# Kernel optimization log

Measured on AMD Instinct MI355X. Metric: run time of the kernel, lower is better.

Reference implementation:

```python
import jax, jax.numpy as jnp
import numpy as np

B, IMG, P, CIN = 4, 384, 16, 3
G = IMG // P            # 24 patches per side
NP = G * G              # 576 patch tokens
N = NP + 1              # +cls
D, H, L, MLP, NC = 768, 12, 12, 3072, 1000
HD = D // H
SCALE = HD ** -0.5
NUM_REL = (2 * G - 1) * (2 * G - 1) + 3   # (2*1-1)*(2G-1)*(2G-1)+3 = 2212
EPS = 1e-6


def gen_rel_index():
    # window (1, G, G): depth diff is always 0, reduces to 2D BEiT indexing
    coords = np.stack(np.meshgrid(np.arange(G), np.arange(G), indexing='ij')).reshape(2, -1)
    rel = (coords[:, :, None] - coords[:, None, :]).transpose(1, 2, 0).copy()  # (NP,NP,2)
    rel[:, :, 0] += G - 1
    rel[:, :, 1] += G - 1
    rel[:, :, 0] *= 2 * G - 1
    idx = np.zeros((N, N), dtype=np.int32)
    idx[1:, 1:] = rel.sum(-1)
    idx[0, :] = NUM_REL - 3
    idx[:, 0] = NUM_REL - 2
    idx[0, 0] = NUM_REL - 1
    return jnp.asarray(idx)


def setup_inputs() -> dict:
    key = jax.random.key(0)
    ks = jax.random.split(key, 20)
    s = 0.02
    inp = {
        'x': jax.random.normal(ks[0], (B, CIN, IMG, IMG), jnp.float32),
        'patch_w': s * jax.random.normal(ks[1], (D, CIN * P * P), jnp.float32),
        'patch_b': jnp.zeros((D,), jnp.float32),
        'cls_token': s * jax.random.normal(ks[2], (1, 1, D), jnp.float32),
        'pos_embed': s * jax.random.normal(ks[3], (1, N, D), jnp.float32),
        'ln1_w': jnp.ones((L, D), jnp.float32),
        'ln1_b': jnp.zeros((L, D), jnp.float32),
        'qkv_w': s * jax.random.normal(ks[4], (L, 3 * D, D), jnp.float32),
        'q_bias': jnp.zeros((L, D), jnp.float32),
        'v_bias': jnp.zeros((L, D), jnp.float32),
        'proj_w': s * jax.random.normal(ks[5], (L, D, D), jnp.float32),
        'proj_b': jnp.zeros((L, D), jnp.float32),
        'ln2_w': jnp.ones((L, D), jnp.float32),
        'ln2_b': jnp.zeros((L, D), jnp.float32),
        'fc1_w': s * jax.random.normal(ks[6], (L, MLP, D), jnp.float32),
        'fc1_b': jnp.zeros((L, MLP), jnp.float32),
        'fc2_w': s * jax.random.normal(ks[7], (L, D, MLP), jnp.float32),
        'fc2_b': jnp.zeros((L, D), jnp.float32),
        'rel_table': s * jax.random.normal(ks[8], (L, NUM_REL, H), jnp.float32),
        'fc_norm_w': jnp.ones((D,), jnp.float32),
        'fc_norm_b': jnp.zeros((D,), jnp.float32),
        'head_w': s * jax.random.normal(ks[9], (NC, D), jnp.float32),
        'head_b': jnp.zeros((NC,), jnp.float32),
        'rel_index': gen_rel_index(),
    }
    return inp


def _ln(x, w, b):
    m = x.mean(-1, keepdims=True)
    v = ((x - m) ** 2).mean(-1, keepdims=True)
    return (x - m) * jax.lax.rsqrt(v + EPS) * w + b


def _beit_fwd(x, patch_w, patch_b, cls_token, pos_embed,
              ln1_w, ln1_b, qkv_w, q_bias, v_bias, proj_w, proj_b,
              ln2_w, ln2_b, fc1_w, fc1_b, fc2_w, fc2_b, rel_table,
              fc_norm_w, fc_norm_b, head_w, head_b, rel_index):
    # patch embed: conv P x P stride P == reshape + matmul; patch vec order (c, ph, pw)
    patches = x.reshape(B, CIN, G, P, G, P).transpose(0, 2, 4, 1, 3, 5).reshape(B, NP, CIN * P * P)
    tok = patches @ patch_w.T + patch_b                      # (B, NP, D)
    h = jnp.concatenate([jnp.broadcast_to(cls_token, (B, 1, D)), tok], axis=1) + pos_embed

    def block(h, p):
        l1w, l1b, qw, qb, vb, pw, pb, l2w, l2b, f1w, f1b, f2w, f2b, rt = p
        y = _ln(h, l1w, l1b)
        bias = jnp.concatenate([qb, jnp.zeros_like(qb), vb])  # k_bias frozen zeros
        qkv = (y @ qw.T + bias).reshape(B, N, 3, H, HD).transpose(2, 0, 3, 1, 4)
        q, k, v = qkv[0] * SCALE, qkv[1], qkv[2]              # (B,H,N,HD)
        attn = jnp.einsum('bhnd,bhmd->bhnm', q, k)
        rel = rt[rel_index].transpose(2, 0, 1)                # (H,N,N)
        attn = jax.nn.softmax(attn + rel[None], axis=-1)
        o = jnp.einsum('bhnm,bhmd->bhnd', attn, v).transpose(0, 2, 1, 3).reshape(B, N, D)
        h = h + (o @ pw.T + pb)
        y = _ln(h, l2w, l2b)
        y = jax.nn.gelu(y @ f1w.T + f1b, approximate=False) @ f2w.T + f2b
        return h + y, None

    xs = (ln1_w, ln1_b, qkv_w, q_bias, v_bias, proj_w, proj_b,
          ln2_w, ln2_b, fc1_w, fc1_b, fc2_w, fc2_b, rel_table)
    h, _ = jax.lax.scan(block, h, xs)

    pooled = h[:, 1:].mean(axis=1)                            # global_pool='avg' drops cls
    return _ln(pooled, fc_norm_w, fc_norm_b) @ head_w.T + head_b  # (B, NC)


def reference(x, patch_w, patch_b, cls_token, pos_embed,
              ln1_w, ln1_b, qkv_w, q_bias, v_bias, proj_w, proj_b,
              ln2_w, ln2_b, fc1_w, fc1_b, fc2_w, fc2_b, rel_table,
              fc_norm_w, fc_norm_b, head_w, head_b, rel_index):
    return _beit_fwd(x, patch_w, patch_b, cls_token, pos_embed,
                     ln1_w, ln1_b, qkv_w, q_bias, v_bias, proj_w, proj_b,
                     ln2_w, ln2_b, fc1_w, fc1_b, fc2_w, fc2_b, rel_table,
                     fc_norm_w, fc_norm_b, head_w, head_b, rel_index)
```

## Files before the change

kernel.cpp:

```cpp
#include <hip/hip_runtime.h>
#include <math.h>

typedef unsigned short u16;
typedef __bf16 bf16x8_t __attribute__((ext_vector_type(8)));
typedef u16 u16x8 __attribute__((ext_vector_type(8)));
typedef float f32x4 __attribute__((ext_vector_type(4)));

#define CBATCH 4
#define CN 577
#define CNP 576
#define CD 768
#define CH 12
#define CHD 64
#define CL 12
#define CMLP 3072
#define CVP 640
#define CROWS (CBATCH*CN)
#define CROWSP 2432
#define CNN2 332929
#define CBH (CBATCH*CH)
#define CSK 4
#define CMT 37

__device__ __forceinline__ float b2f(u16 u){
  unsigned x = ((unsigned)u) << 16;
  return __builtin_bit_cast(float, x);
}
__device__ __forceinline__ u16 f2b(float f){
  unsigned x = __builtin_bit_cast(unsigned, f);
  unsigned r = x + 0x7fffu + ((x >> 16) & 1u);
  return (u16)(r >> 16);
}

__device__ __forceinline__ f32x4 MFMA(u16x8 a, u16x8 b, f32x4 c){
  return __builtin_amdgcn_mfma_f32_16x16x32_bf16(
      __builtin_bit_cast(bf16x8_t, a), __builtin_bit_cast(bf16x8_t, b), c, 0, 0, 0);
}

__device__ __forceinline__ void gl_lds16(const u16* g, u16* l){
  __builtin_amdgcn_global_load_lds(
      (const __attribute__((address_space(1))) unsigned int*)g,
      (__attribute__((address_space(3))) unsigned int*)l, 16, 0, 0);
}


__global__ void cvt_kernel(const float* __restrict__ src, u16* __restrict__ dst, int n){
  int i = (blockIdx.x * 256 + threadIdx.x) * 4;
  if(i < n){
    float4 v = *reinterpret_cast<const float4*>(src + i);
    ushort4 o;
    o.x = f2b(v.x); o.y = f2b(v.y); o.z = f2b(v.z); o.w = f2b(v.w);
    *reinterpret_cast<ushort4*>(dst + i) = o;
  }
}

__global__ void zero_kernel(u16* __restrict__ p, int n){
  int i = (blockIdx.x * 256 + threadIdx.x) * 8;
  if(i < n){
    u16x8 z = {0,0,0,0,0,0,0,0};
    *reinterpret_cast<u16x8*>(p + i) = z;
  }
}

__global__ void im2col_kernel(const float* __restrict__ x, u16* __restrict__ out){
  int id = blockIdx.x * 256 + threadIdx.x;
  if(id >= 2304*768) return;
  int col = id % 768, row = id / 768;
  int b = row / 576, p = row % 576;
  int gy = p / 24, gx = p % 24;
  int c = col >> 8, rem = col & 255, py = rem >> 4, px = rem & 15;
  float v = x[(((long)(b*3 + c)*384) + gy*16 + py)*384 + gx*16 + px];
  out[id] = f2b(v);
}

__global__ void clspos_kernel(const float* __restrict__ cls, const float* __restrict__ pos,
                              float* __restrict__ h){
  int id = blockIdx.x * 256 + threadIdx.x;
  if(id < CBATCH*CD){
    int b = id / CD, d = id % CD;
    h[(long)b*CN*CD + d] = cls[d] + pos[d];
  }
}

template<bool BF16OUT>
__global__ void ln_kernel(const float* __restrict__ x, const float* __restrict__ w,
                          const float* __restrict__ bsh, u16* __restrict__ yb,
                          float* __restrict__ yf){
  int r = blockIdx.x;
  int tid = threadIdx.x;
  const float* px = x + (long)r*CD;
  float v0 = px[tid], v1 = px[tid+256], v2 = px[tid+512];
  __shared__ float red[4];
  float s = v0 + v1 + v2;
  #pragma unroll
  for(int m=1;m<64;m<<=1) s += __shfl_xor(s, m);
  if((tid & 63) == 0) red[tid>>6] = s;
  __syncthreads();
  s = red[0]+red[1]+red[2]+red[3];
  float mean = s * (1.0f/768.0f);
  float d0 = v0-mean, d1 = v1-mean, d2 = v2-mean;
  float s2 = d0*d0 + d1*d1 + d2*d2;
  __syncthreads();
  #pragma unroll
  for(int m=1;m<64;m<<=1) s2 += __shfl_xor(s2, m);
  if((tid & 63) == 0) red[tid>>6] = s2;
  __syncthreads();
  s2 = red[0]+red[1]+red[2]+red[3];
  float rs = rsqrtf(s2*(1.0f/768.0f) + 1e-6f);
  float o0 = d0*rs*w[tid]     + bsh[tid];
  float o1 = d1*rs*w[tid+256] + bsh[tid+256];
  float o2 = d2*rs*w[tid+512] + bsh[tid+512];
  if(BF16OUT){
    yb[(long)r*CD + tid]     = f2b(o0);
    yb[(long)r*CD + tid+256] = f2b(o1);
    yb[(long)r*CD + tid+512] = f2b(o2);
  } else {
    yf[(long)r*CD + tid]     = o0;
    yf[(long)r*CD + tid+256] = o1;
    yf[(long)r*CD + tid+512] = o2;
  }
}

template<bool DOLN>
__global__ void resid_ln_kernel(float* __restrict__ h, const float* __restrict__ part,
    const float* __restrict__ bias, const float* __restrict__ w,
    const float* __restrict__ bsh, u16* __restrict__ y){
  int r = blockIdx.x, tid = threadIdx.x;
  float v[3];
  #pragma unroll
  for(int j=0;j<3;j++){
    int c = tid + j*256;
    float t = h[(long)r*CD + c] + bias[c];
    #pragma unroll
    for(int sk=0; sk<CSK; sk++) t += part[((long)sk*CROWS + r)*CD + c];
    v[j] = t;
    h[(long)r*CD + c] = t;
  }
  if constexpr(DOLN){
    __shared__ float red[4];
    float s = v[0]+v[1]+v[2];
    #pragma unroll
    for(int m=1;m<64;m<<=1) s += __shfl_xor(s, m);
    if((tid & 63) == 0) red[tid>>6] = s;
    __syncthreads();
    s = red[0]+red[1]+red[2]+red[3];
    float mean = s * (1.0f/768.0f);
    float d0=v[0]-mean, d1=v[1]-mean, d2=v[2]-mean;
    float s2 = d0*d0+d1*d1+d2*d2;
    __syncthreads();
    #pragma unroll
    for(int m=1;m<64;m<<=1) s2 += __shfl_xor(s2, m);
    if((tid & 63) == 0) red[tid>>6] = s2;
    __syncthreads();
    s2 = red[0]+red[1]+red[2]+red[3];
    float rs = rsqrtf(s2*(1.0f/768.0f) + 1e-6f);
    y[(long)r*CD + tid]     = f2b(d0*rs*w[tid]     + bsh[tid]);
    y[(long)r*CD + tid+256] = f2b(d1*rs*w[tid+256] + bsh[tid+256]);
    y[(long)r*CD + tid+512] = f2b(d2*rs*w[tid+512] + bsh[tid+512]);
  }
}

__global__ void relbias_all_kernel(const int* __restrict__ ridx, const float* __restrict__ rtab,
                                   u16* __restrict__ attb){
  int id = blockIdx.x * 256 + threadIdx.x;
  if(id >= CNN2) return;
  int l = blockIdx.y;
  int idx = ridx[id];
  const float* rowp = rtab + (long)l*2212*12 + (long)idx*12;
  u16* dst = attb + (long)l*12*CNN2;
  #pragma unroll
  for(int hh=0; hh<12; hh++)
    dst[(long)hh*CNN2 + id] = f2b(rowp[hh]);
}

__global__ __launch_bounds__(256) void attn_kernel(
    const u16* __restrict__ q, const u16* __restrict__ k,
    const u16* __restrict__ vt, const u16* __restrict__ attb,
    u16* __restrict__ o_){
  __shared__ u16 pt[4][16*72];
  const int tid = threadIdx.x, lane = tid & 63, wv = tid >> 6;
  const int i15 = lane & 15, g4 = lane >> 4;
  const int qt = blockIdx.x, bh = blockIdx.y;
  const int b = bh / CH, hh = bh % CH;
  const int qrow0 = qt*64 + wv*16;
  const u16* qp = q + ((long)bh*CN + qrow0 + i15)*CHD + g4*8;
  u16x8 qa0 = *reinterpret_cast<const u16x8*>(qp);
  u16x8 qa1 = *reinterpret_cast<const u16x8*>(qp + 32);
  const u16* kbase = k + (long)bh*CN*CHD;
  const u16* vbase = vt + (long)bh*CHD*CVP;
  const u16* bb = attb + (long)hh*CNN2;
  f32x4 po[4];
  float m[4], l[4];
  #pragma unroll
  for(int i=0;i<4;i++){ po[i]=(f32x4){0,0,0,0}; m[i]=-3.0e38f; l[i]=0.0f; }

  for(int t=0;t<10;t++){
    const int kv0 = t*64;
    f32x4 sa[4];
    #pragma unroll
    for(int fc=0;fc<4;fc++){
      const u16* kp = kbase + ((long)(kv0 + fc*16 + i15))*CHD + g4*8;
      u16x8 k0 = *reinterpret_cast<const u16x8*>(kp);
      u16x8 k1 = *reinterpret_cast<const u16x8*>(kp + 32);
      f32x4 z = (f32x4){0,0,0,0};
      z = MFMA(qa0, k0, z);
      z = MFMA(qa1, k1, z);
      sa[fc] = z;
    }
    float s[4][4];
    #pragma unroll
    for(int fc=0;fc<4;fc++){
      int kvc = kv0 + fc*16 + i15;
      bool valid = kvc < CN;
      #pragma unroll
      for(int r=0;r<4;r++){
        int qr = qrow0 + g4*4 + r;
        float bias = b2f(bb[(long)qr*CN + kvc]);
        s[fc][r] = valid ? (sa[fc][r] + bias) : -1e30f;
      }
    }
    float tm[4], ts[4], sc[4];
    #pragma unroll
    for(int r=0;r<4;r++)
      tm[r] = fmaxf(fmaxf(s[0][r],s[1][r]), fmaxf(s[2][r],s[3][r]));
    #pragma unroll
    for(int msk=1; msk<16; msk<<=1)
      #pragma unroll
      for(int r=0;r<4;r++)
        tm[r] = fmaxf(tm[r], __shfl_xor(tm[r], msk));
    #pragma unroll
    for(int r=0;r<4;r++){
      float mn = fmaxf(m[r], tm[r]);
      sc[r] = exp2f((m[r]-mn)*1.4426950408889634f);
      m[r] = mn;
      ts[r] = 0.f;
    }
    #pragma unroll
    for(int fc=0;fc<4;fc++)
      #pragma unroll
      for(int r=0;r<4;r++){
        float p = exp2f((s[fc][r]-m[r])*1.4426950408889634f);
        s[fc][r] = p; ts[r] += p;
      }
    #pragma unroll
    for(int msk=1; msk<16; msk<<=1)
      #pragma unroll
      for(int r=0;r<4;r++)
        ts[r] += __shfl_xor(ts[r], msk);
    #pragma unroll
    for(int r=0;r<4;r++) l[r] = l[r]*sc[r] + ts[r];
    #pragma unroll
    for(int d=0; d<4; d++)
      #pragma unroll
      for(int r=0;r<4;r++) po[d][r] *= sc[r];
    #pragma unroll
    for(int fc=0;fc<4;fc++)
      #pragma unroll
      for(int r=0;r<4;r++)
        pt[wv][(g4*4+r)*72 + fc*16 + i15] = f2b(s[fc][r]);
    u16x8 pa0 = *reinterpret_cast<const u16x8*>(&pt[wv][i15*72 + g4*8]);
    u16x8 pa1 = *reinterpret_cast<const u16x8*>(&pt[wv][i15*72 + 32 + g4*8]);
    #pragma unroll
    for(int d=0; d<4; d++){
      const u16* vp = vbase + ((long)(d*16 + i15))*CVP + kv0 + g4*8;
      u16x8 v0 = *reinterpret_cast<const u16x8*>(vp);
      u16x8 v1 = *reinterpret_cast<const u16x8*>(vp + 32);
      po[d] = MFMA(pa0, v0, po[d]);
      po[d] = MFMA(pa1, v1, po[d]);
    }
  }
  #pragma unroll
  for(int d=0; d<4; d++)
    #pragma unroll
    for(int r=0;r<4;r++){
      int qr = qrow0 + g4*4 + r;
      if(qr < CN)
        o_[((long)(b*CN + qr))*CD + hh*CHD + d*16 + i15] = f2b(po[d][r] / l[r]);
    }
}

__global__ void pool_kernel(const float* __restrict__ h, float* __restrict__ pooled){
  int id = blockIdx.x * 256 + threadIdx.x;
  if(id >= CBATCH*CD) return;
  int b = id / CD, d = id % CD;
  const float* p = h + ((long)b*CN + 1)*CD + d;
  float s = 0.0f;
  for(int i=0;i<CNP;i++) s += p[(long)i*CD];
  pooled[id] = s * (1.0f/576.0f);
}

__global__ void head_kernel(const float* __restrict__ xn, const float* __restrict__ hw,
                            const float* __restrict__ hb, float* __restrict__ out){
  int nc = blockIdx.x;
  int tid = threadIdx.x;
  const float* wr = hw + (long)nc*CD;
  float w0 = wr[tid], w1 = wr[tid+256], w2 = wr[tid+512];
  __shared__ float red[4];
  for(int b=0;b<CBATCH;b++){
    const float* xr = xn + (long)b*CD;
    float s = w0*xr[tid] + w1*xr[tid+256] + w2*xr[tid+512];
    #pragma unroll
    for(int m=1;m<64;m<<=1) s += __shfl_xor(s, m);
    if((tid&63)==0) red[tid>>6] = s;
    __syncthreads();
    if(tid==0) out[b*1000 + nc] = red[0]+red[1]+red[2]+red[3] + hb[nc];
    __syncthreads();
  }
}


struct EpiArgs {
  float* hres;
  u16* outb;
  const float* bias;
  const float* pos;
  const float* qb;
  const float* vb;
  u16* q;
  u16* k;
  u16* vt;
  float* part;
};

enum { EPI_PATCH=0, EPI_QKV, EPI_GELU, EPI_PART };

template<int EPI>
__global__ __launch_bounds__(256,4) void gemm4(const u16* __restrict__ A, const u16* __restrict__ Bm,
    int M, int N, int K, int lda, int ldb, EpiArgs e){
  __shared__ __align__(16) u16 lA[3][64*32];
  __shared__ __align__(16) u16 lB[3][128*32];
  const int tid  = threadIdx.x;
  const int lane = tid & 63;
  const int wv   = tid >> 6;

  const int bm = blockIdx.y * 64, bn = blockIdx.x * 128;
  const int z  = blockIdx.z;
  A  += (long)z * K;
  Bm += (long)z * K;

  const int srow = wv*16 + (lane>>2);
  const u16* Asb = A  + (long)(bm + srow)*lda + (lane&3)*8;
  const u16* Bsb = Bm + (long)(bn + srow)*ldb + (lane&3)*8;
  const int ldst = wv*16*32;

  const int rbase = (wv>>1)*32;
  const int cbase = (wv&1)*64;
  const int i15 = lane & 15;
  const int k8off = (lane>>4)<<3;

  f32x4 acc[2][4];
  #pragma unroll
  for(int i=0;i<2;i++)
    #pragma unroll
    for(int j=0;j<4;j++)
      acc[i][j] = (f32x4){0.0f,0.0f,0.0f,0.0f};

  const int nkt = K >> 5;

  auto STAGE = [&](int kt, int slot){
    const u16* Ak = Asb + (long)kt*32;
    const u16* Bk = Bsb + (long)kt*32;
    gl_lds16(Ak,          &lA[slot][ldst]);
    gl_lds16(Bk,          &lB[slot][ldst]);
    gl_lds16(Bk + 64*ldb, &lB[slot][ldst + 64*32]);
  };

  STAGE(0, 0);
  if(nkt > 1) STAGE(1, 1);

  for(int kt=0; kt<nkt; kt++){
    if(kt+1 < nkt) asm volatile("s_waitcnt vmcnt(3) lgkmcnt(0)" ::: "memory");
    else           asm volatile("s_waitcnt vmcnt(0) lgkmcnt(0)" ::: "memory");
    __builtin_amdgcn_s_barrier();
    int nxt2 = kt + 2; 
    if(nxt2 < nkt){ int sl = nxt2 % 3; STAGE(nxt2, sl); }
    const int cur = kt % 3;
    u16x8 af[2], bfr[4];
    #pragma unroll
    for(int f=0; f<2; f++)
      af[f]  = *reinterpret_cast<const u16x8*>(&lA[cur][(rbase + f*16 + i15)*32 + k8off]);
    #pragma unroll
    for(int f=0; f<4; f++)
      bfr[f] = *reinterpret_cast<const u16x8*>(&lB[cur][(cbase + f*16 + i15)*32 + k8off]);
    #pragma unroll
    for(int fr=0; fr<2; fr++)
      #pragma unroll
      for(int fc=0; fc<4; fc++)
        acc[fr][fc] = MFMA(af[fr], bfr[fc], acc[fr][fc]);
  }

  #pragma unroll
  for(int fr=0; fr<2; fr++){
    #pragma unroll
    for(int fc=0; fc<4; fc++){
      #pragma unroll
      for(int r=0;r<4;r++){
        int row = bm + rbase + fr*16 + ((lane>>4)<<2) + r;
        int col = bn + cbase + fc*16 + i15;
        if(row >= M || col >= N) continue;
        float v = acc[fr][fc][r];
        if constexpr(EPI == EPI_PATCH){
          int b = row/576, p = row%576;
          e.hres[((long)b*CN + 1 + p)*CD + col] = v + e.bias[col] + e.pos[(long)(1+p)*CD + col];
        } else if constexpr(EPI == EPI_QKV){
          int b = row/CN, n = row%CN;
          if(col < 768){
            int hh = col>>6, d = col&63;
            e.q[(((long)(b*CH+hh))*CN + n)*CHD + d] = f2b((v + e.qb[col]) * 0.125f);
          } else if(col < 1536){
            int c2 = col-768; int hh = c2>>6, d = c2&63;
            e.k[(((long)(b*CH+hh))*CN + n)*CHD + d] = f2b(v);
          } else {
            int c2 = col-1536; int hh = c2>>6, d = c2&63;
            e.vt[(((long)(b*CH+hh))*CHD + d)*CVP + n] = f2b(v + e.vb[c2]);
          }
        } else if constexpr(EPI == EPI_GELU){
          float t = v + e.bias[col];
          e.outb[(long)row*N + col] = f2b(t * 0.5f * (1.0f + erff(t*0.70710678118f)));
        } else {
          e.part[((long)z*CROWS + row)*CD + col] = v;
        }
      }
    }
  }
}


extern "C" void kernel_launch(void* const* d_in, const int* in_sizes, int n_in,
                              void* d_out, int out_size, void* d_ws, size_t ws_size,
                              hipStream_t stream){
  const float* x        = (const float*)d_in[0];
  const float* patch_w  = (const float*)d_in[1];
  const float* patch_b  = (const float*)d_in[2];
  const float* cls_tok  = (const float*)d_in[3];
  const float* pos_emb  = (const float*)d_in[4];
  const float* ln1_w    = (const float*)d_in[5];
  const float* ln1_b    = (const float*)d_in[6];
  const float* qkv_w    = (const float*)d_in[7];
  const float* q_bias   = (const float*)d_in[8];
  const float* v_bias   = (const float*)d_in[9];
  const float* proj_w   = (const float*)d_in[10];
  const float* proj_b   = (const float*)d_in[11];
  const float* ln2_w    = (const float*)d_in[12];
  const float* ln2_b    = (const float*)d_in[13];
  const float* fc1_w    = (const float*)d_in[14];
  const float* fc1_b    = (const float*)d_in[15];
  const float* fc2_w    = (const float*)d_in[16];
  const float* fc2_b    = (const float*)d_in[17];
  const float* rel_tab  = (const float*)d_in[18];
  const float* fcn_w    = (const float*)d_in[19];
  const float* fcn_b    = (const float*)d_in[20];
  const float* head_w   = (const float*)d_in[21];
  const float* head_b   = (const float*)d_in[22];
  const int*   rel_idx  = (const int*)d_in[23];
  float* out = (float*)d_out;
  char* ws = (char*)d_ws;

  size_t off = 0;
  auto alloc = [&](size_t bytes)->size_t{
    size_t o = off; off += (bytes + 255) & ~(size_t)255; return o;
  };
  const size_t OFF_H    = alloc((size_t)CROWS*CD*4);
  const size_t OFF_Y    = alloc((size_t)CROWSP*CD*2);
  const size_t OFF_Q    = alloc(((size_t)CBH*CN + 64)*CHD*2);
  const size_t OFF_K    = alloc(((size_t)CBH*CN + 64)*CHD*2);
  const size_t OFF_VT   = alloc((size_t)CBH*CHD*CVP*2);
  const size_t OFF_O    = alloc((size_t)CROWSP*CD*2);
  const size_t OFF_HID  = alloc((size_t)CROWSP*CMLP*2);
  const size_t OFF_PART = alloc((size_t)CSK*CROWS*CD*4);
  const size_t OFF_ATTB = alloc(((size_t)CL*CH*CNN2 + 64*1024)*2);
  const size_t OFF_WP0  = alloc((size_t)768*768*2);
  const size_t OFF_WQA  = alloc((size_t)CL*2304*768*2);
  const size_t OFF_WPA  = alloc((size_t)CL*768*768*2);
  const size_t OFF_W1A  = alloc((size_t)CL*3072*768*2);
  const size_t OFF_W2A  = alloc((size_t)CL*768*3072*2);
  const size_t OFF_PL   = alloc((size_t)CBATCH*CD*4);
  const size_t OFF_NM   = alloc((size_t)CBATCH*CD*4);
  (void)ws_size; (void)in_sizes; (void)n_in; (void)out_size;

  float* h      = (float*)(ws + OFF_H);
  u16*   y      = (u16*)(ws + OFF_Y);
  u16*   qb_    = (u16*)(ws + OFF_Q);
  u16*   kb_    = (u16*)(ws + OFF_K);
  u16*   vt_    = (u16*)(ws + OFF_VT);
  u16*   o_     = (u16*)(ws + OFF_O);
  u16*   hid    = (u16*)(ws + OFF_HID);
  float* part   = (float*)(ws + OFF_PART);
  u16*   attb   = (u16*)(ws + OFF_ATTB);
  u16*   wp0    = (u16*)(ws + OFF_WP0);
  u16*   wqA    = (u16*)(ws + OFF_WQA);
  u16*   wpA    = (u16*)(ws + OFF_WPA);
  u16*   w1A    = (u16*)(ws + OFF_W1A);
  u16*   w2A    = (u16*)(ws + OFF_W2A);
  float* pooled = (float*)(ws + OFF_PL);
  float* normed = (float*)(ws + OFF_NM);

  auto cvt = [&](const float* src, u16* dst, long n){
    cvt_kernel<<<dim3((unsigned)((n/4 + 255)/256)), dim3(256), 0, stream>>>(src, dst, (int)n);
  };

  {
    int n = CBH*CHD*CVP;
    zero_kernel<<<dim3((n/8 + 255)/256), dim3(256), 0, stream>>>(vt_, n);
  }
  im2col_kernel<<<dim3((2304*768 + 255)/256), dim3(256), 0, stream>>>(x, hid);
  cvt(patch_w, wp0, 768*768);
  cvt(qkv_w,  wqA, (long)CL*2304*768);
  cvt(proj_w, wpA, (long)CL*768*768);
  cvt(fc1_w,  w1A, (long)CL*3072*768);
  cvt(fc2_w,  w2A, (long)CL*768*3072);
  relbias_all_kernel<<<dim3((CNN2 + 255)/256, CL), dim3(256), 0, stream>>>(
      rel_idx, rel_tab, attb);

  {
    EpiArgs e{}; e.hres = h; e.bias = patch_b; e.pos = pos_emb;
    gemm4<EPI_PATCH><<<dim3(6,36,1), dim3(256), 0, stream>>>(
        hid, wp0, 2304, 768, 768, 768, 768, e);
  }
  clspos_kernel<<<dim3(12), dim3(256), 0, stream>>>(cls_tok, pos_emb, h);

  ln_kernel<true><<<dim3(CROWS), dim3(256), 0, stream>>>(
      h, ln1_w, ln1_b, y, nullptr);

  for(int l=0; l<CL; l++){
    {
      EpiArgs e{}; e.qb = q_bias + l*CD; e.vb = v_bias + l*CD;
      e.q = qb_; e.k = kb_; e.vt = vt_;
      gemm4<EPI_QKV><<<dim3(18,CMT,1), dim3(256), 0, stream>>>(
          y, wqA + (long)l*2304*768, CROWS, 2304, 768, 768, 768, e);
    }
    attn_kernel<<<dim3(10, CBH), dim3(256), 0, stream>>>(
        qb_, kb_, vt_, attb + (long)l*CH*CNN2, o_);
    {
      EpiArgs e{}; e.part = part;
      gemm4<EPI_PART><<<dim3(6,CMT,CSK), dim3(256), 0, stream>>>(
          o_, wpA + (long)l*768*768, CROWS, 768, 768/CSK, 768, 768, e);
    }
    resid_ln_kernel<true><<<dim3(CROWS), dim3(256), 0, stream>>>(
        h, part, proj_b + l*CD, ln2_w + l*CD, ln2_b + l*CD, y);
    {
      EpiArgs e{}; e.outb = hid; e.bias = fc1_b + l*CMLP;
      gemm4<EPI_GELU><<<dim3(24,CMT,1), dim3(256), 0, stream>>>(
          y, w1A + (long)l*3072*768, CROWS, 3072, 768, 768, 768, e);
    }
    {
      EpiArgs e{}; e.part = part;
      gemm4<EPI_PART><<<dim3(6,CMT,CSK), dim3(256), 0, stream>>>(
          hid, w2A + (long)l*768*3072, CROWS, 768, 3072/CSK, 3072, 3072, e);
    }
    if(l+1 < CL){
      resid_ln_kernel<true><<<dim3(CROWS), dim3(256), 0, stream>>>(
          h, part, fc2_b + l*CD, ln1_w + (l+1)*CD, ln1_b + (l+1)*CD, y);
    } else {
      resid_ln_kernel<false><<<dim3(CROWS), dim3(256), 0, stream>>>(
          h, part, fc2_b + l*CD, nullptr, nullptr, nullptr);
    }
  }

  pool_kernel<<<dim3(12), dim3(256), 0, stream>>>(h, pooled);
  ln_kernel<false><<<dim3(CBATCH), dim3(256), 0, stream>>>(
      pooled, fcn_w, fcn_b, nullptr, normed);
  head_kernel<<<dim3(1000), dim3(256), 0, stream>>>(normed, head_w, head_b, out);
}
```

Before: 2.162 ms.

## Stage attention K/V tiles through double-buffered LDS and halve split-K count

The attention kernel now cooperatively loads each 64-key K tile and V^T tile into double-buffered shared memory with async global-to-LDS copies, prefetching the next tile while computing the current one. Previously each wave read K and V directly from global memory, so the four waves in a block fetched the same data redundantly. This adds two block barriers per iteration and more LDS use per block. Separately, the split-K factor CSK drops from 4 to 2, and the Q/K buffers get extra padding so the last staged tile stays in bounds.

```diff
diff --git a/kernel.cpp b/kernel.cpp
--- a/kernel.cpp
+++ b/kernel.cpp
@@ -19,7 +19,7 @@
 #define CROWSP 2432
 #define CNN2 332929
 #define CBH (CBATCH*CH)
-#define CSK 4
+#define CSK 2
 #define CMT 37
 
 __device__ __forceinline__ float b2f(u16 u){
@@ -177,6 +177,8 @@
     const u16* __restrict__ q, const u16* __restrict__ k,
     const u16* __restrict__ vt, const u16* __restrict__ attb,
     u16* __restrict__ o_){
+  __shared__ __align__(16) u16 lK[2][64*64];
+  __shared__ __align__(16) u16 lV[2][64*64];
   __shared__ u16 pt[4][16*72];
   const int tid = threadIdx.x, lane = tid & 63, wv = tid >> 6;
   const int i15 = lane & 15, g4 = lane >> 4;
@@ -189,19 +191,42 @@
   const u16* kbase = k + (long)bh*CN*CHD;
   const u16* vbase = vt + (long)bh*CHD*CVP;
   const u16* bb = attb + (long)hh*CNN2;
+
+  const int srow = wv*16 + (lane>>3);
+  const int scol = (lane&7)*8;
+  const int sdst = wv*16*64;
+
   f32x4 po[4];
   float m[4], l[4];
   #pragma unroll
   for(int i=0;i<4;i++){ po[i]=(f32x4){0,0,0,0}; m[i]=-3.0e38f; l[i]=0.0f; }
 
+  auto STAGE = [&](int t, int buf){
+    const int kv0 = t*64;
+    const u16* ks = kbase + ((long)(kv0 + srow))*CHD + scol;
+    const u16* vs = vbase + ((long)srow)*CVP + kv0 + scol;
+    gl_lds16(ks,          &lK[buf][sdst]);
+    gl_lds16(ks + 8*CHD,  &lK[buf][sdst + 8*64]);
+    gl_lds16(vs,          &lV[buf][sdst]);
+    gl_lds16(vs + 8*CVP,  &lV[buf][sdst + 8*64]);
+  };
+
+  STAGE(0, 0);
   for(int t=0;t<10;t++){
+    if(t+1 < 10){
+      STAGE(t+1, (t+1)&1);
+      asm volatile("s_waitcnt vmcnt(4)" ::: "memory");
+    } else {
+      asm volatile("s_waitcnt vmcnt(0)" ::: "memory");
+    }
+    __syncthreads();
+    const int buf = t&1;
     const int kv0 = t*64;
     f32x4 sa[4];
     #pragma unroll
     for(int fc=0;fc<4;fc++){
-      const u16* kp = kbase + ((long)(kv0 + fc*16 + i15))*CHD + g4*8;
-      u16x8 k0 = *reinterpret_cast<const u16x8*>(kp);
-      u16x8 k1 = *reinterpret_cast<const u16x8*>(kp + 32);
+      u16x8 k0 = *reinterpret_cast<const u16x8*>(&lK[buf][(fc*16+i15)*64 + g4*8]);
+      u16x8 k1 = *reinterpret_cast<const u16x8*>(&lK[buf][(fc*16+i15)*64 + 32 + g4*8]);
       f32x4 z = (f32x4){0,0,0,0};
       z = MFMA(qa0, k0, z);
       z = MFMA(qa1, k1, z);
@@ -262,12 +287,12 @@
     u16x8 pa1 = *reinterpret_cast<const u16x8*>(&pt[wv][i15*72 + 32 + g4*8]);
     #pragma unroll
     for(int d=0; d<4; d++){
-      const u16* vp = vbase + ((long)(d*16 + i15))*CVP + kv0 + g4*8;
-      u16x8 v0 = *reinterpret_cast<const u16x8*>(vp);
-      u16x8 v1 = *reinterpret_cast<const u16x8*>(vp + 32);
+      u16x8 v0 = *reinterpret_cast<const u16x8*>(&lV[buf][(d*16+i15)*64 + g4*8]);
+      u16x8 v1 = *reinterpret_cast<const u16x8*>(&lV[buf][(d*16+i15)*64 + 32 + g4*8]);
       po[d] = MFMA(pa0, v0, po[d]);
       po[d] = MFMA(pa1, v1, po[d]);
     }
+    __syncthreads();
   }
   #pragma unroll
   for(int d=0; d<4; d++)
@@ -372,7 +397,7 @@
     if(kt+1 < nkt) asm volatile("s_waitcnt vmcnt(3) lgkmcnt(0)" ::: "memory");
     else           asm volatile("s_waitcnt vmcnt(0) lgkmcnt(0)" ::: "memory");
     __builtin_amdgcn_s_barrier();
-    int nxt2 = kt + 2; 
+    int nxt2 = kt + 2;
     if(nxt2 < nkt){ int sl = nxt2 % 3; STAGE(nxt2, sl); }
     const int cur = kt % 3;
     u16x8 af[2], bfr[4];
@@ -462,8 +487,8 @@
   };
   const size_t OFF_H    = alloc((size_t)CROWS*CD*4);
   const size_t OFF_Y    = alloc((size_t)CROWSP*CD*2);
-  const size_t OFF_Q    = alloc(((size_t)CBH*CN + 64)*CHD*2);
-  const size_t OFF_K    = alloc(((size_t)CBH*CN + 64)*CHD*2);
+  const size_t OFF_Q    = alloc(((size_t)CBH*CN + 128)*CHD*2);
+  const size_t OFF_K    = alloc(((size_t)CBH*CN + 128)*CHD*2);
   const size_t OFF_VT   = alloc((size_t)CBH*CHD*CVP*2);
   const size_t OFF_O    = alloc((size_t)CROWSP*CD*2);
   const size_t OFF_HID  = alloc((size_t)CROWSP*CMLP*2);
```

New measurement: 2.097 ms. 3.0% less time.
